# Kernel optimization log

Hardware: AMD Instinct MI355X
Metric: run time of the kernel (lower is better)

Reference implementation:

```python
import jax, jax.numpy as jnp
import numpy as np

IN_FEATURES = 1024
NUM_HEADS = 16
DIM = IN_FEATURES // NUM_HEADS  # 64
CONV_OUT = 10
B, T = 32, 2048


def setup_inputs() -> dict:
    key = jax.random.key(0)
    ks = jax.random.split(key, 10)
    inp = {
        "query": jax.random.normal(ks[0], (B, 1, IN_FEATURES), dtype=jnp.float32),
        "value": jax.random.normal(ks[1], (B, T, IN_FEATURES), dtype=jnp.float32),
        "prev_align": jax.random.uniform(ks[2], (B, NUM_HEADS, T), dtype=jnp.float32),
        # parameters (torch nn.Linear weight layout: (out, in))
        "Wq": jax.random.normal(ks[3], (NUM_HEADS * DIM, IN_FEATURES), dtype=jnp.float32) * 0.02,
        "Wv": jax.random.normal(ks[4], (NUM_HEADS * DIM, IN_FEATURES), dtype=jnp.float32) * 0.02,
        "conv_w": jax.random.normal(ks[5], (CONV_OUT, NUM_HEADS, 3), dtype=jnp.float32) * 0.1,
        "conv_b": jax.random.normal(ks[6], (CONV_OUT,), dtype=jnp.float32) * 0.1,
        "Wu": jax.random.normal(ks[7], (DIM, CONV_OUT), dtype=jnp.float32) * 0.1,
        "bias": jax.random.uniform(ks[8], (DIM,), dtype=jnp.float32, minval=-0.1, maxval=0.1),
        "score_w": jax.random.normal(ks[9], (1, DIM), dtype=jnp.float32) * 0.1,
        "score_b": jnp.zeros((1,), dtype=jnp.float32),
    }
    return inp


def reference(query, value, prev_align, Wq, Wv, conv_w, conv_b, Wu, bias, score_w, score_b):
    batch, seq_len = value.shape[0], value.shape[1]
    H, d = prev_align.shape[1], Wu.shape[0]

    # location features: Conv1d(H -> C_out, k=3, pad=1) over time, then Linear(C_out -> d), tanh
    conv = jax.lax.conv_general_dilated(
        prev_align, conv_w, window_strides=(1,), padding=((1, 1),),
        dimension_numbers=("NCW", "OIW", "NCW"))  # (B, C_out, T)
    conv = conv + conv_b[None, :, None]
    loc_energy = jnp.tanh(jnp.einsum("bct,dc->btd", conv, Wu))  # (B, T, d)

    # projections, split into heads
    q = jnp.einsum("bqf,ef->bqe", query, Wq).reshape(batch, 1, H, d).transpose(0, 2, 1, 3)  # (B,H,1,d)
    v = jnp.einsum("btf,ef->bte", value, Wv).reshape(batch, seq_len, H, d).transpose(0, 2, 1, 3)  # (B,H,T,d)

    # additive energy: broadcast sum + tanh, then dim->1 scoring
    e = jnp.tanh(v + q + loc_energy[:, None, :, :] + bias)  # (B,H,T,d)
    score = jnp.einsum("bhtd,d->bht", e, score_w[0]) + score_b[0]  # (B,H,T)
    align = jax.nn.softmax(score, axis=-1)  # (B,H,T)

    context = jnp.einsum("bht,bhtd->bhd", align, v).reshape(batch, 1, H * d)  # (B,1,H*d)
    return context, align
```

## Files before the change

### kernel.cpp

```cpp
#include <hip/hip_runtime.h>
#include <stdint.h>
#include <stddef.h>

#define B_ 32
#define T_ 2048
#define F_ 1024
#define H_ 16
#define D_ 64
#define C_ 10

typedef __bf16 bf16;
typedef __bf16 bf16x8 __attribute__((ext_vector_type(8)));
typedef float f32x4 __attribute__((ext_vector_type(4)));

#define GLD_LDS16(g, l)                                                        \
  __builtin_amdgcn_global_load_lds(                                            \
      (const __attribute__((address_space(1))) void*)(g),                      \
      (__attribute__((address_space(3))) void*)(l), 16, 0, 0)

__device__ __forceinline__ float tanh_fast(float x) {
  float e = __expf(2.f * x);
  return 1.f - 2.f / (e + 1.f);
}

__global__ __launch_bounds__(256) void k_cvt_bf16(const float* __restrict__ src,
                                                  bf16* __restrict__ dst, int n) {
  int i = (blockIdx.x * 256 + threadIdx.x) * 8;
  if (i + 8 <= n) {
    float4 a = *reinterpret_cast<const float4*>(src + i);
    float4 b = *reinterpret_cast<const float4*>(src + i + 4);
    bf16x8 o;
    o[0] = (bf16)a.x; o[1] = (bf16)a.y; o[2] = (bf16)a.z; o[3] = (bf16)a.w;
    o[4] = (bf16)b.x; o[5] = (bf16)b.y; o[6] = (bf16)b.z; o[7] = (bf16)b.w;
    *reinterpret_cast<bf16x8*>(dst + i) = o;
  }
}

__global__ __launch_bounds__(256) void k_prep(const float* __restrict__ Wu,
                                              const float* __restrict__ cw,
                                              const float* __restrict__ cb,
                                              float* __restrict__ W2T,
                                              float* __restrict__ B2) {
  int tid = threadIdx.x;
  for (int idx = tid; idx < H_ * 3 * D_; idx += 256) {
    int d = idx & 63;
    int hk = idx >> 6;
    int h = hk / 3, k = hk % 3;
    float s = 0.f;
    for (int c = 0; c < C_; c++) s += Wu[d * C_ + c] * cw[c * H_ * 3 + h * 3 + k];
    W2T[idx] = s;
  }
  if (tid < D_) {
    float s = 0.f;
    for (int c = 0; c < C_; c++) s += Wu[tid * C_ + c] * cb[c];
    B2[tid] = s;
  }
}

__global__ __launch_bounds__(256) void k_q(const float* __restrict__ query,
                                           const float* __restrict__ Wq,
                                           const float* __restrict__ bias,
                                           float* __restrict__ qv) {
  int gw = blockIdx.x * 4 + (threadIdx.x >> 6);
  int lane = threadIdx.x & 63;
  int b = gw >> 10, e = gw & 1023;
  const float* qr = query + (size_t)b * F_;
  const float* wr = Wq + (size_t)e * F_;
  float s = 0.f;
  for (int i = lane; i < F_; i += 64) s += qr[i] * wr[i];
  for (int off = 32; off; off >>= 1) s += __shfl_xor(s, off);
  if (lane == 0) qv[(size_t)b * F_ + e] = s + bias[e & 63];
}

__global__ __launch_bounds__(256) void k_loc(const float* __restrict__ pa,
                                             const float* __restrict__ W2T,
                                             const float* __restrict__ B2,
                                             float* __restrict__ loc) {
  int blk = blockIdx.x;
  int b = blk >> 9;
  int t0 = (blk & 511) * 4;
  __shared__ float sW[H_ * 3 * D_];
  __shared__ float spa[H_][8];
  __shared__ float sB2[D_];
  int tid = threadIdx.x;
  for (int i = tid; i < H_ * 3 * D_; i += 256) sW[i] = W2T[i];
  if (tid < 96) {
    int h = tid / 6, j = tid % 6;
    int t = t0 - 1 + j;
    spa[h][j] = (t >= 0 && t < T_) ? pa[((size_t)b * H_ + h) * T_ + t] : 0.f;
  }
  if (tid < D_) sB2[tid] = B2[tid];
  __syncthreads();
  int tl = tid >> 6, d = tid & 63;
  float s = sB2[d];
#pragma unroll
  for (int h = 0; h < H_; h++)
#pragma unroll
    for (int k = 0; k < 3; k++)
      s += spa[h][tl + k] * sW[(h * 3 + k) * 64 + d];
  loc[((size_t)b * T_ + t0 + tl) * 64 + d] = tanh_fast(s);
}

__global__ __launch_bounds__(256, 4) void k_score(const bf16* __restrict__ vbf,
                                                  const bf16* __restrict__ wbf,
                                                  const float* __restrict__ qv,
                                                  const float* __restrict__ loc,
                                                  const float* __restrict__ sw,
                                                  float* __restrict__ score) {
  int wg = blockIdx.x;
  int swz = (wg & 7) * 1024 + (wg >> 3);
  int mtile = swz >> 4, h = swz & 15;
  int bb = mtile >> 4;
  int t0 = (mtile & 15) << 7;

  __shared__ __align__(16) bf16 As[128 * 64];
  __shared__ __align__(16) bf16 Bs[64 * 64];

  int tid = threadIdx.x;
  int w = tid >> 6, l = tid & 63;
  const bf16* Ag = vbf + ((size_t)bb * T_ + t0) * F_;
  const bf16* Bg = wbf + ((size_t)h * 64) * F_;
  int kswz = 8 * ((l & 7) ^ (l >> 3));
  int rsub = l >> 3;

  f32x4 acc[2][4] = {};

  for (int kt = 0; kt < 16; kt++) {
    int kbase = kt * 64;
#pragma unroll
    for (int j = 0; j < 4; j++) {
      int c = w * 4 + j;
      const bf16* g = Ag + ((size_t)(c * 8 + rsub)) * F_ + kbase + kswz;
      GLD_LDS16(g, As + c * 512);
    }
#pragma unroll
    for (int j = 0; j < 2; j++) {
      int c = w * 2 + j;
      const bf16* g = Bg + ((size_t)(c * 8 + rsub)) * F_ + kbase + kswz;
      GLD_LDS16(g, Bs + c * 512);
    }
    __syncthreads();

    int r = l & 15, g4 = l >> 4;
#pragma unroll
    for (int kk = 0; kk < 2; kk++) {
      bf16x8 a[2], bb_[4];
#pragma unroll
      for (int rt = 0; rt < 2; rt++) {
        int row = w * 32 + rt * 16 + r;
        int byte = row * 128 + (((kk * 4 + g4) ^ (row & 7)) << 4);
        a[rt] = *(const bf16x8*)((const char*)As + byte);
      }
#pragma unroll
      for (int ct = 0; ct < 4; ct++) {
        int e = ct * 16 + r;
        int byte = e * 128 + (((kk * 4 + g4) ^ (e & 7)) << 4);
        bb_[ct] = *(const bf16x8*)((const char*)Bs + byte);
      }
#pragma unroll
      for (int rt = 0; rt < 2; rt++)
#pragma unroll
        for (int ct = 0; ct < 4; ct++)
          acc[rt][ct] = __builtin_amdgcn_mfma_f32_16x16x32_bf16(
              a[rt], bb_[ct], acc[rt][ct], 0, 0, 0);
    }
    __syncthreads();
  }

  int r = l & 15, g4 = l >> 4;
  float qq[4], swv[4];
#pragma unroll
  for (int ct = 0; ct < 4; ct++) {
    int d = ct * 16 + r;
    qq[ct] = qv[(size_t)bb * F_ + h * 64 + d];
    swv[ct] = sw[d];
  }
#pragma unroll
  for (int rt = 0; rt < 2; rt++) {
#pragma unroll
    for (int rr = 0; rr < 4; rr++) {
      int trow = t0 + w * 32 + rt * 16 + g4 * 4 + rr;
      const float* lrow = loc + ((size_t)bb * T_ + trow) * 64;
      float p = 0.f;
#pragma unroll
      for (int ct = 0; ct < 4; ct++) {
        float x = acc[rt][ct][rr] + qq[ct] + lrow[ct * 16 + r];
        p += tanh_fast(x) * swv[ct];
      }
      p += __shfl_xor(p, 1);
      p += __shfl_xor(p, 2);
      p += __shfl_xor(p, 4);
      p += __shfl_xor(p, 8);
      if (r == 0)
        score[((size_t)bb * H_ + h) * T_ + trow] = p;
    }
  }
}

__global__ __launch_bounds__(256) void k_softmax(const float* __restrict__ score,
                                                 float* __restrict__ align) {
  int bh = blockIdx.x;
  const float* s = score + (size_t)bh * T_;
  float* a = align + (size_t)bh * T_;
  int tid = threadIdx.x;
  float v[8];
  float m = -1e30f;
#pragma unroll
  for (int j = 0; j < 8; j++) {
    v[j] = s[tid + j * 256];
    m = fmaxf(m, v[j]);
  }
  for (int off = 32; off; off >>= 1) m = fmaxf(m, __shfl_xor(m, off));
  __shared__ float red[4], red2[4];
  int w = tid >> 6, l = tid & 63;
  if (l == 0) red[w] = m;
  __syncthreads();
  m = fmaxf(fmaxf(red[0], red[1]), fmaxf(red[2], red[3]));
  float sum = 0.f;
#pragma unroll
  for (int j = 0; j < 8; j++) {
    v[j] = __expf(v[j] - m);
    sum += v[j];
  }
  for (int off = 32; off; off >>= 1) sum += __shfl_xor(sum, off);
  if (l == 0) red2[w] = sum;
  __syncthreads();
  sum = red2[0] + red2[1] + red2[2] + red2[3];
  float inv = 1.f / sum;
#pragma unroll
  for (int j = 0; j < 8; j++) a[tid + j * 256] = v[j] * inv;
}

__global__ __launch_bounds__(256) void k_upart(const float* __restrict__ value,
                                               const float* __restrict__ align,
                                               float* __restrict__ upart) {
  int blk = blockIdx.x;
  int tc = blk >> 7, b = (blk >> 2) & 31, fc = blk & 3;
  int tid = threadIdx.x;
  int f = fc * 256 + tid;
  __shared__ float sal[256][17];
  for (int idx = tid; idx < 256 * 16; idx += 256) {
    int hh = idx >> 8, tl = idx & 255;
    sal[tl][hh] = align[((size_t)b * H_ + hh) * T_ + tc * 256 + tl];
  }
  __syncthreads();
  float u[16];
#pragma unroll
  for (int h = 0; h < 16; h++) u[h] = 0.f;
  const float* vp = value + ((size_t)b * T_ + tc * 256) * F_ + f;
#pragma unroll 4
  for (int tl = 0; tl < 256; tl++) {
    float x = vp[(size_t)tl * F_];
#pragma unroll
    for (int h = 0; h < 16; h++) u[h] = fmaf(sal[tl][h], x, u[h]);
  }
#pragma unroll
  for (int h = 0; h < 16; h++)
    upart[(((size_t)tc * B_ + b) * H_ + h) * F_ + f] = u[h];
}

__global__ __launch_bounds__(256) void k_context(const float* __restrict__ upart,
                                                 const float* __restrict__ Wv,
                                                 float* __restrict__ ctx) {
  int bh = blockIdx.x;
  int b = bh >> 4, h = bh & 15;
  int tid = threadIdx.x;
  __shared__ float su[1024];
  for (int j = 0; j < 4; j++) {
    int f = tid + j * 256;
    float s = 0.f;
    for (int tc = 0; tc < 8; tc++)
      s += upart[(((size_t)tc * B_ + b) * H_ + h) * F_ + f];
    su[f] = s;
  }
  __syncthreads();
  int d = tid >> 2, part = tid & 3;
  const float* wr = Wv + ((size_t)(h * 64 + d)) * F_ + part * 256;
  float s = 0.f;
  for (int i = 0; i < 256; i++) s += su[part * 256 + i] * wr[i];
  s += __shfl_xor(s, 1);
  s += __shfl_xor(s, 2);
  if (part == 0) ctx[(size_t)b * F_ + h * 64 + d] = s;
}

extern "C" void kernel_launch(void* const* d_in, const int* in_sizes, int n_in,
                              void* d_out, int out_size, void* d_ws, size_t ws_size,
                              hipStream_t stream) {
  const float* query      = (const float*)d_in[0];
  const float* value      = (const float*)d_in[1];
  const float* prev_align = (const float*)d_in[2];
  const float* Wq         = (const float*)d_in[3];
  const float* Wv         = (const float*)d_in[4];
  const float* conv_w     = (const float*)d_in[5];
  const float* conv_b     = (const float*)d_in[6];
  const float* Wu         = (const float*)d_in[7];
  const float* bias       = (const float*)d_in[8];
  const float* score_w    = (const float*)d_in[9];

  char* ws = (char*)d_ws;
  bf16*  vbf   = (bf16*)(ws + 0);
  bf16*  wbf   = (bf16*)(ws + 134217728);
  float* qv    = (float*)(ws + 136314880);
  float* loc   = (float*)(ws + 136445952);
  float* W2T   = (float*)(ws + 153223168);
  float* B2    = (float*)(ws + 153235456);
  float* score = (float*)(ws + 153235712);
  float* upart = (float*)(ws + 0);

  float* ctx   = (float*)d_out;
  float* align = (float*)d_out + 32768;

  k_cvt_bf16<<<32768, 256, 0, stream>>>(value, vbf, B_ * T_ * F_);
  k_cvt_bf16<<<512, 256, 0, stream>>>(Wv, wbf, F_ * F_);
  k_prep<<<1, 256, 0, stream>>>(Wu, conv_w, conv_b, W2T, B2);
  k_q<<<8192, 256, 0, stream>>>(query, Wq, bias, qv);
  k_loc<<<B_ * T_ / 4, 256, 0, stream>>>(prev_align, W2T, B2, loc);
  k_score<<<8192, 256, 0, stream>>>(vbf, wbf, qv, loc, score_w, score);
  k_softmax<<<B_ * H_, 256, 0, stream>>>(score, align);
  k_upart<<<1024, 256, 0, stream>>>(value, align, upart);
  k_context<<<B_ * H_, 256, 0, stream>>>(upart, Wv, ctx);
}
```

Baseline: 748.1 us.

## Widen score tile to two heads, batch query projection, vectorize upart

```diff
diff --git a/kernel.cpp b/kernel.cpp
--- a/kernel.cpp
+++ b/kernel.cpp
@@ -61,15 +61,30 @@
                                            const float* __restrict__ Wq,
                                            const float* __restrict__ bias,
                                            float* __restrict__ qv) {
-  int gw = blockIdx.x * 4 + (threadIdx.x >> 6);
-  int lane = threadIdx.x & 63;
-  int b = gw >> 10, e = gw & 1023;
-  const float* qr = query + (size_t)b * F_;
+  int e = blockIdx.x;
+  __shared__ float swq[F_];
+  int tid = threadIdx.x;
   const float* wr = Wq + (size_t)e * F_;
-  float s = 0.f;
-  for (int i = lane; i < F_; i += 64) s += qr[i] * wr[i];
-  for (int off = 32; off; off >>= 1) s += __shfl_xor(s, off);
-  if (lane == 0) qv[(size_t)b * F_ + e] = s + bias[e & 63];
+  for (int i = tid; i < F_; i += 256) swq[i] = wr[i];
+  __syncthreads();
+  int w = tid >> 6, l = tid & 63;
+  float s[8];
+#pragma unroll
+  for (int j = 0; j < 8; j++) s[j] = 0.f;
+  for (int i = l; i < F_; i += 64) {
+    float wv = swq[i];
+#pragma unroll
+    for (int j = 0; j < 8; j++)
+      s[j] += query[(size_t)(w * 8 + j) * F_ + i] * wv;
+  }
+#pragma unroll
+  for (int j = 0; j < 8; j++)
+    for (int off = 32; off; off >>= 1) s[j] += __shfl_xor(s[j], off);
+  if (l == 0) {
+    float bb = bias[e & 63];
+#pragma unroll
+    for (int j = 0; j < 8; j++) qv[(size_t)(w * 8 + j) * F_ + e] = s[j] + bb;
+  }
 }
 
 __global__ __launch_bounds__(256) void k_loc(const float* __restrict__ pa,
@@ -101,50 +116,48 @@
   loc[((size_t)b * T_ + t0 + tl) * 64 + d] = tanh_fast(s);
 }
 
-__global__ __launch_bounds__(256, 4) void k_score(const bf16* __restrict__ vbf,
+__global__ __launch_bounds__(256, 3) void k_score(const bf16* __restrict__ vbf,
                                                   const bf16* __restrict__ wbf,
                                                   const float* __restrict__ qv,
                                                   const float* __restrict__ loc,
                                                   const float* __restrict__ sw,
                                                   float* __restrict__ score) {
   int wg = blockIdx.x;
-  int swz = (wg & 7) * 1024 + (wg >> 3);
-  int mtile = swz >> 4, h = swz & 15;
+  int swz = (wg & 7) * 512 + (wg >> 3);
+  int mtile = swz >> 3, hp = swz & 7;
   int bb = mtile >> 4;
   int t0 = (mtile & 15) << 7;
 
   __shared__ __align__(16) bf16 As[128 * 64];
-  __shared__ __align__(16) bf16 Bs[64 * 64];
+  __shared__ __align__(16) bf16 Bs[128 * 64];
 
   int tid = threadIdx.x;
   int w = tid >> 6, l = tid & 63;
   const bf16* Ag = vbf + ((size_t)bb * T_ + t0) * F_;
-  const bf16* Bg = wbf + ((size_t)h * 64) * F_;
+  const bf16* Bg = wbf + ((size_t)hp * 128) * F_;
   int kswz = 8 * ((l & 7) ^ (l >> 3));
   int rsub = l >> 3;
 
-  f32x4 acc[2][4] = {};
+  f32x4 acc[2][8] = {};
 
   for (int kt = 0; kt < 16; kt++) {
     int kbase = kt * 64;
 #pragma unroll
     for (int j = 0; j < 4; j++) {
       int c = w * 4 + j;
-      const bf16* g = Ag + ((size_t)(c * 8 + rsub)) * F_ + kbase + kswz;
-      GLD_LDS16(g, As + c * 512);
-    }
-#pragma unroll
-    for (int j = 0; j < 2; j++) {
-      int c = w * 2 + j;
-      const bf16* g = Bg + ((size_t)(c * 8 + rsub)) * F_ + kbase + kswz;
-      GLD_LDS16(g, Bs + c * 512);
+      GLD_LDS16(Ag + ((size_t)(c * 8 + rsub)) * F_ + kbase + kswz, As + c * 512);
+    }
+#pragma unroll
+    for (int j = 0; j < 4; j++) {
+      int c = w * 4 + j;
+      GLD_LDS16(Bg + ((size_t)(c * 8 + rsub)) * F_ + kbase + kswz, Bs + c * 512);
     }
     __syncthreads();
 
     int r = l & 15, g4 = l >> 4;
 #pragma unroll
     for (int kk = 0; kk < 2; kk++) {
-      bf16x8 a[2], bb_[4];
+      bf16x8 a[2], bq[8];
 #pragma unroll
       for (int rt = 0; rt < 2; rt++) {
         int row = w * 32 + rt * 16 + r;
@@ -152,28 +165,28 @@
         a[rt] = *(const bf16x8*)((const char*)As + byte);
       }
 #pragma unroll
-      for (int ct = 0; ct < 4; ct++) {
+      for (int ct = 0; ct < 8; ct++) {
         int e = ct * 16 + r;
         int byte = e * 128 + (((kk * 4 + g4) ^ (e & 7)) << 4);
-        bb_[ct] = *(const bf16x8*)((const char*)Bs + byte);
+        bq[ct] = *(const bf16x8*)((const char*)Bs + byte);
       }
 #pragma unroll
       for (int rt = 0; rt < 2; rt++)
 #pragma unroll
-        for (int ct = 0; ct < 4; ct++)
+        for (int ct = 0; ct < 8; ct++)
           acc[rt][ct] = __builtin_amdgcn_mfma_f32_16x16x32_bf16(
-              a[rt], bb_[ct], acc[rt][ct], 0, 0, 0);
+              a[rt], bq[ct], acc[rt][ct], 0, 0, 0);
     }
     __syncthreads();
   }
 
   int r = l & 15, g4 = l >> 4;
-  float qq[4], swv[4];
-#pragma unroll
-  for (int ct = 0; ct < 4; ct++) {
-    int d = ct * 16 + r;
-    qq[ct] = qv[(size_t)bb * F_ + h * 64 + d];
-    swv[ct] = sw[d];
+  float qq[8], swv[8];
+#pragma unroll
+  for (int ct = 0; ct < 8; ct++) {
+    int el = ct * 16 + r;
+    qq[ct] = qv[(size_t)bb * F_ + hp * 128 + el];
+    swv[ct] = sw[el & 63];
   }
 #pragma unroll
   for (int rt = 0; rt < 2; rt++) {
@@ -181,18 +194,23 @@
     for (int rr = 0; rr < 4; rr++) {
       int trow = t0 + w * 32 + rt * 16 + g4 * 4 + rr;
       const float* lrow = loc + ((size_t)bb * T_ + trow) * 64;
-      float p = 0.f;
+      float lv[4];
+#pragma unroll
+      for (int j = 0; j < 4; j++) lv[j] = lrow[j * 16 + r];
+      float p0 = 0.f, p1 = 0.f;
 #pragma unroll
       for (int ct = 0; ct < 4; ct++) {
-        float x = acc[rt][ct][rr] + qq[ct] + lrow[ct * 16 + r];
-        p += tanh_fast(x) * swv[ct];
+        p0 += tanh_fast(acc[rt][ct][rr] + qq[ct] + lv[ct]) * swv[ct];
+        p1 += tanh_fast(acc[rt][ct + 4][rr] + qq[ct + 4] + lv[ct]) * swv[ct + 4];
       }
-      p += __shfl_xor(p, 1);
-      p += __shfl_xor(p, 2);
-      p += __shfl_xor(p, 4);
-      p += __shfl_xor(p, 8);
-      if (r == 0)
-        score[((size_t)bb * H_ + h) * T_ + trow] = p;
+      p0 += __shfl_xor(p0, 1); p1 += __shfl_xor(p1, 1);
+      p0 += __shfl_xor(p0, 2); p1 += __shfl_xor(p1, 2);
+      p0 += __shfl_xor(p0, 4); p1 += __shfl_xor(p1, 4);
+      p0 += __shfl_xor(p0, 8); p1 += __shfl_xor(p1, 8);
+      if (r == 0) {
+        score[((size_t)bb * H_ + hp * 2) * T_ + trow] = p0;
+        score[((size_t)bb * H_ + hp * 2 + 1) * T_ + trow] = p1;
+      }
     }
   }
 }
@@ -235,28 +253,35 @@
                                                const float* __restrict__ align,
                                                float* __restrict__ upart) {
   int blk = blockIdx.x;
-  int tc = blk >> 7, b = (blk >> 2) & 31, fc = blk & 3;
-  int tid = threadIdx.x;
-  int f = fc * 256 + tid;
+  int tc = blk >> 6, b = (blk >> 1) & 31, fc = blk & 1;
+  int tid = threadIdx.x;
+  int f = fc * 512 + tid * 2;
   __shared__ float sal[256][17];
   for (int idx = tid; idx < 256 * 16; idx += 256) {
     int hh = idx >> 8, tl = idx & 255;
     sal[tl][hh] = align[((size_t)b * H_ + hh) * T_ + tc * 256 + tl];
   }
   __syncthreads();
-  float u[16];
-#pragma unroll
-  for (int h = 0; h < 16; h++) u[h] = 0.f;
+  float ux[16], uy[16];
+#pragma unroll
+  for (int h = 0; h < 16; h++) { ux[h] = 0.f; uy[h] = 0.f; }
   const float* vp = value + ((size_t)b * T_ + tc * 256) * F_ + f;
 #pragma unroll 4
   for (int tl = 0; tl < 256; tl++) {
-    float x = vp[(size_t)tl * F_];
-#pragma unroll
-    for (int h = 0; h < 16; h++) u[h] = fmaf(sal[tl][h], x, u[h]);
-  }
-#pragma unroll
-  for (int h = 0; h < 16; h++)
-    upart[(((size_t)tc * B_ + b) * H_ + h) * F_ + f] = u[h];
+    float2 x = *reinterpret_cast<const float2*>(vp + (size_t)tl * F_);
+#pragma unroll
+    for (int h = 0; h < 16; h++) {
+      float al = sal[tl][h];
+      ux[h] = fmaf(al, x.x, ux[h]);
+      uy[h] = fmaf(al, x.y, uy[h]);
+    }
+  }
+#pragma unroll
+  for (int h = 0; h < 16; h++) {
+    float2 o; o.x = ux[h]; o.y = uy[h];
+    *reinterpret_cast<float2*>(
+        &upart[(((size_t)tc * B_ + b) * H_ + h) * F_ + f]) = o;
+  }
 }
 
 __global__ __launch_bounds__(256) void k_context(const float* __restrict__ upart,
@@ -313,10 +338,10 @@
   k_cvt_bf16<<<32768, 256, 0, stream>>>(value, vbf, B_ * T_ * F_);
   k_cvt_bf16<<<512, 256, 0, stream>>>(Wv, wbf, F_ * F_);
   k_prep<<<1, 256, 0, stream>>>(Wu, conv_w, conv_b, W2T, B2);
-  k_q<<<8192, 256, 0, stream>>>(query, Wq, bias, qv);
+  k_q<<<1024, 256, 0, stream>>>(query, Wq, bias, qv);
   k_loc<<<B_ * T_ / 4, 256, 0, stream>>>(prev_align, W2T, B2, loc);
-  k_score<<<8192, 256, 0, stream>>>(vbf, wbf, qv, loc, score_w, score);
+  k_score<<<4096, 256, 0, stream>>>(vbf, wbf, qv, loc, score_w, score);
   k_softmax<<<B_ * H_, 256, 0, stream>>>(score, align);
-  k_upart<<<1024, 256, 0, stream>>>(value, align, upart);
+  k_upart<<<512, 256, 0, stream>>>(value, align, upart);
   k_context<<<B_ * H_, 256, 0, stream>>>(upart, Wv, ctx);
 }
```

Measured after the change: 743.9 us. About the same (-0.6%).
